# Kernel tuning notes

Hardware: AMD Instinct MI355X
Metric: run time of the kernel (lower is better)

## Reference

```python
import jax, jax.numpy as jnp
import numpy as np

N = 50000          # nodes
E = 800000         # directed edges (avg degree 16)
IN_F = 1433        # Cora num_features
N_CLS = 7          # Cora num_classes
HEADS = 8
HID = 32
NEG_SLOPE = 0.2    # PyG GATConv default negative_slope


def gat_conv(x, src, dst, W, a_src, a_dst, bias, heads, out_ch):
    """PyG GATConv (concat=True, add_self_loops=True, eval mode)."""
    n = x.shape[0]
    h = (x @ W).reshape(n, heads, out_ch)            # [N, H, C]
    # add self loops (PyG default)
    loop = jnp.arange(n, dtype=src.dtype)
    src = jnp.concatenate([src, loop])
    dst = jnp.concatenate([dst, loop])
    # attention logits per edge: a_src . h_src + a_dst . h_dst
    alpha_src = (h * a_src).sum(-1)                  # [N, H]
    alpha_dst = (h * a_dst).sum(-1)                  # [N, H]
    e = jax.nn.leaky_relu(alpha_src[src] + alpha_dst[dst], NEG_SLOPE)  # [E+N, H]
    # segment softmax over incoming edges of each destination node
    m = jax.ops.segment_max(e, dst, num_segments=n)  # [N, H]
    p = jnp.exp(e - m[dst])
    denom = jax.ops.segment_sum(p, dst, num_segments=n)
    alpha = p / denom[dst]                           # [E+N, H]
    # attention-weighted scatter-aggregate of source features
    out = jax.ops.segment_sum(h[src] * alpha[:, :, None], dst, num_segments=n)  # [N, H, C]
    return out.reshape(n, heads * out_ch) + bias


def setup_inputs() -> dict:
    key = jax.random.key(0)
    ks = jax.random.split(key, 12)
    s = 0.05
    x = jax.random.normal(ks[0], (N, IN_F), dtype=jnp.float32)
    edge_index = jax.random.randint(ks[1], (2, E), 0, N, dtype=jnp.int32)
    W1 = jax.random.normal(ks[2], (IN_F, HEADS * HID), dtype=jnp.float32) * s
    att_src1 = jax.random.normal(ks[3], (HEADS, HID), dtype=jnp.float32) * s
    att_dst1 = jax.random.normal(ks[4], (HEADS, HID), dtype=jnp.float32) * s
    bias1 = jnp.zeros((HEADS * HID,), dtype=jnp.float32)
    W2 = jax.random.normal(ks[5], (HEADS * HID, HEADS * N_CLS), dtype=jnp.float32) * s
    att_src2 = jax.random.normal(ks[6], (HEADS, N_CLS), dtype=jnp.float32) * s
    att_dst2 = jax.random.normal(ks[7], (HEADS, N_CLS), dtype=jnp.float32) * s
    bias2 = jnp.zeros((HEADS * N_CLS,), dtype=jnp.float32)
    return {
        "x": x, "edge_index": edge_index,
        "W1": W1, "att_src1": att_src1, "att_dst1": att_dst1, "bias1": bias1,
        "W2": W2, "att_src2": att_src2, "att_dst2": att_dst2, "bias2": bias2,
    }


def reference(x, edge_index, W1, att_src1, att_dst1, bias1,
              W2, att_src2, att_dst2, bias2):
    src, dst = edge_index[0], edge_index[1]
    # dropout (p=0.6) is identity in eval mode
    h = gat_conv(x, src, dst, W1, att_src1, att_dst1, bias1, HEADS, HID)
    h = jax.nn.elu(h)
    out = gat_conv(h, src, dst, W2, att_src2, att_dst2, bias2, HEADS, N_CLS)
    return out  # [N, HEADS * N_CLS]
```

## Files before the change

### kernel.cpp

```cpp
#include <hip/hip_runtime.h>
#include <math.h>

typedef short s16x8 __attribute__((ext_vector_type(8)));
typedef float f32x4 __attribute__((ext_vector_type(4)));

#define SLOPE 0.2f
#define K1 1433
#define KP 1440
#define NKB 45

static __device__ __forceinline__ float leaky(float x) {
  return x > 0.f ? x : SLOPE * x;
}

static __device__ __forceinline__ unsigned short f2bf(float f) {
  unsigned u = __builtin_bit_cast(unsigned, f);
  u += 0x7FFFu + ((u >> 16) & 1u);
  return (unsigned short)(u >> 16);
}
static __device__ __forceinline__ float bf2f(unsigned short h) {
  unsigned u = ((unsigned)h) << 16;
  return __builtin_bit_cast(float, u);
}

__global__ void w1t_kernel(const float* __restrict__ W1,
                           unsigned short* __restrict__ w1f) {
  int tid = blockIdx.x * 256 + threadIdx.x;
  if (tid >= NKB * 16 * 64) return;
  int l = tid & 63;
  int chunk = tid >> 6;
  int ntg = chunk & 15;
  int kb = chunk >> 4;
  int n = ntg * 16 + (l & 15);
  int kbase = kb * 32 + (l >> 4) * 8;
  unsigned short o[8];
#pragma unroll
  for (int e = 0; e < 8; ++e) {
    int k = kbase + e;
    float v = (k < K1) ? W1[(long)k * 256 + n] : 0.f;
    o[e] = f2bf(v);
  }
  *(ulonglong2*)(w1f + (long)tid * 8) = *(ulonglong2*)o;
}

__global__ __launch_bounds__(256, 3) void gemm1_mfma_kernel(
    const float* __restrict__ A, const unsigned short* __restrict__ w1f,
    float* __restrict__ C, int M) {
  __shared__ unsigned short As[2][4 * 2 * 64 * 8];
  __shared__ unsigned short Bs[2][16 * 64 * 8];
  const int t = threadIdx.x;
  const int w = t >> 6, l = t & 63;
  const int row0 = blockIdx.x * 64;

  f32x4 acc[4][4];
#pragma unroll
  for (int mt = 0; mt < 4; ++mt)
#pragma unroll
    for (int nt = 0; nt < 4; ++nt)
#pragma unroll
      for (int r = 0; r < 4; ++r) acc[mt][nt][r] = 0.f;

  const int sr = t >> 2, sg = t & 3;
  const int smt = sr >> 4, slr = sr & 15;
  const int lane_dst = slr + 16 * sg;
  const bool rowok = (row0 + sr) < M;
  const float* arow = A + (long)(row0 + sr) * K1;

  float v[8];

#pragma unroll
  for (int q = 0; q < 4; ++q) {
    int ng = w * 4 + q;
    const unsigned short* gsrc = w1f + (((long)0 * 16 + ng) * 64 + l) * 8;
    unsigned short* ldst = &Bs[0][ng * 512];
    __builtin_amdgcn_global_load_lds(
        (const __attribute__((address_space(1))) unsigned int*)gsrc,
        (__attribute__((address_space(3))) unsigned int*)ldst, 16, 0, 0);
  }
  {
    int kbase = sg * 8;
#pragma unroll
    for (int i = 0; i < 8; ++i) {
      int gk = kbase + i;
      v[i] = (rowok && gk < K1) ? arow[gk] : 0.f;
    }
    unsigned short hv[8], lv[8];
#pragma unroll
    for (int e = 0; e < 8; ++e) {
      unsigned short h = f2bf(v[e]);
      hv[e] = h;
      lv[e] = f2bf(v[e] - bf2f(h));
    }
    *(ulonglong2*)&As[0][((smt * 2 + 0) * 64 + lane_dst) * 8] = *(ulonglong2*)hv;
    *(ulonglong2*)&As[0][((smt * 2 + 1) * 64 + lane_dst) * 8] = *(ulonglong2*)lv;
  }
  __syncthreads();

  int cur = 0;
  for (int kb = 0; kb < NKB; ++kb) {
    const int nxt = kb + 1;
    if (nxt < NKB) {
#pragma unroll
      for (int q = 0; q < 4; ++q) {
        int ng = w * 4 + q;
        const unsigned short* gsrc =
            w1f + (((long)nxt * 16 + ng) * 64 + l) * 8;
        unsigned short* ldst = &Bs[cur ^ 1][ng * 512];
        __builtin_amdgcn_global_load_lds(
            (const __attribute__((address_space(1))) unsigned int*)gsrc,
            (__attribute__((address_space(3))) unsigned int*)ldst, 16, 0, 0);
      }
      int kbase = nxt * 32 + sg * 8;
#pragma unroll
      for (int i = 0; i < 8; ++i) {
        int gk = kbase + i;
        v[i] = (rowok && gk < K1) ? arow[gk] : 0.f;
      }
    }
    {
      s16x8 ah[4], al[4], bh[4];
#pragma unroll
      for (int mt = 0; mt < 4; ++mt) {
        ah[mt] = *(const s16x8*)&As[cur][(mt * 2 + 0) * 512 + l * 8];
        al[mt] = *(const s16x8*)&As[cur][(mt * 2 + 1) * 512 + l * 8];
      }
#pragma unroll
      for (int nt = 0; nt < 4; ++nt)
        bh[nt] = *(const s16x8*)&Bs[cur][(w * 4 + nt) * 512 + l * 8];
#pragma unroll
      for (int nt = 0; nt < 4; ++nt)
#pragma unroll
        for (int mt = 0; mt < 4; ++mt) {
          acc[mt][nt] = __builtin_amdgcn_mfma_f32_16x16x32_bf16(
              ah[mt], bh[nt], acc[mt][nt], 0, 0, 0);
          acc[mt][nt] = __builtin_amdgcn_mfma_f32_16x16x32_bf16(
              al[mt], bh[nt], acc[mt][nt], 0, 0, 0);
        }
    }
    if (nxt < NKB) {
      unsigned short hv[8], lv[8];
#pragma unroll
      for (int e = 0; e < 8; ++e) {
        unsigned short h = f2bf(v[e]);
        hv[e] = h;
        lv[e] = f2bf(v[e] - bf2f(h));
      }
      *(ulonglong2*)&As[cur ^ 1][((smt * 2 + 0) * 64 + lane_dst) * 8] =
          *(ulonglong2*)hv;
      *(ulonglong2*)&As[cur ^ 1][((smt * 2 + 1) * 64 + lane_dst) * 8] =
          *(ulonglong2*)lv;
      __syncthreads();
    }
    cur ^= 1;
  }
  const int crow4 = (l >> 4) * 4;
  const int ccol = l & 15;
#pragma unroll
  for (int mt = 0; mt < 4; ++mt) {
#pragma unroll
    for (int r = 0; r < 4; ++r) {
      int grow = row0 + mt * 16 + crow4 + r;
      if (grow < M) {
#pragma unroll
        for (int nt = 0; nt < 4; ++nt) {
          int gcol = w * 64 + nt * 16 + ccol;
          C[(long)grow * 256 + gcol] = acc[mt][nt][r];
        }
      }
    }
  }
}

__global__ void alpha1_kernel(const float* __restrict__ h1,
    const float* __restrict__ a_src, const float* __restrict__ a_dst,
    float* __restrict__ as_o, float* __restrict__ ad_o,
    unsigned short* __restrict__ h1b, int N) {
  int i = blockIdx.x * blockDim.x + threadIdx.x;
  if (i >= N * 8) return;
  int h = i & 7;
  const float* hp = h1 + (long)(i >> 3) * 256 + h * 32;
  const float* sp = a_src + h * 32;
  const float* dp = a_dst + h * 32;
  unsigned short ob[32];
  float s1 = 0.f, s2 = 0.f;
#pragma unroll
  for (int c = 0; c < 32; c += 4) {
    float4 v = *(const float4*)(hp + c);
    float4 ws = *(const float4*)(sp + c);
    float4 wd = *(const float4*)(dp + c);
    s1 += v.x * ws.x + v.y * ws.y + v.z * ws.z + v.w * ws.w;
    s2 += v.x * wd.x + v.y * wd.y + v.z * wd.z + v.w * wd.w;
    ob[c] = f2bf(v.x); ob[c + 1] = f2bf(v.y);
    ob[c + 2] = f2bf(v.z); ob[c + 3] = f2bf(v.w);
  }
  as_o[i] = s1;
  ad_o[i] = s2;
  unsigned short* op = h1b + (long)(i >> 3) * 256 + h * 32;
#pragma unroll
  for (int c = 0; c < 32; c += 8)
    *(ulonglong2*)(op + c) = *(ulonglong2*)(ob + c);
}

__global__ void hist_kernel(const int* __restrict__ dst, int* __restrict__ cnt,
                            int E, int N) {
  int e = blockIdx.x * blockDim.x + threadIdx.x;
  if (e >= E + N) return;
  int d = (e < E) ? dst[e] : (e - E);
  atomicAdd(&cnt[d], 1);
}

__global__ __launch_bounds__(1024) void scan_kernel(
    const int* __restrict__ cnt, int* __restrict__ rowptr,
    int* __restrict__ cursor, int N) {
  __shared__ int part[1024];
  const int tid = threadIdx.x;
  const int chunk = (N + 1023) / 1024;
  const int base = tid * chunk;
  const int lim = min(base + chunk, N);
  int sum = 0;
  for (int i = base; i < lim; ++i) sum += cnt[i];
  part[tid] = sum;
  __syncthreads();
  for (int off = 1; off < 1024; off <<= 1) {
    int v = (tid >= off) ? part[tid - off] : 0;
    __syncthreads();
    part[tid] += v;
    __syncthreads();
  }
  int run = (tid == 0) ? 0 : part[tid - 1];
  for (int i = base; i < lim; ++i) {
    rowptr[i] = run;
    cursor[i] = run;
    run += cnt[i];
  }
  if (tid == 1023) rowptr[N] = part[1023];
}

__global__ void scatter_kernel(const int* __restrict__ src,
    const int* __restrict__ dst, int* __restrict__ cursor,
    int* __restrict__ csr_src, int E, int N) {
  int e = blockIdx.x * blockDim.x + threadIdx.x;
  if (e >= E + N) return;
  int s, d;
  if (e < E) { s = src[e]; d = dst[e]; } else { s = e - E; d = s; }
  int pos = atomicAdd(&cursor[d], 1);
  csr_src[pos] = s;
}

__global__ __launch_bounds__(256) void agg1_fused_kernel(
    const int* __restrict__ rowptr, const int* __restrict__ csr_src,
    const float* __restrict__ as_, const float* __restrict__ ad_,
    const unsigned short* __restrict__ h1b, const float* __restrict__ bias,
    float* __restrict__ act, int N) {
  int d = blockIdx.x * 4 + (threadIdx.x >> 6);
  if (d >= N) return;
  int l = threadIdx.x & 63;
  int h = l >> 3;
  int rs = rowptr[d], re = rowptr[d + 1];
  float adv = ad_[d * 8 + h];
  float4 acc = make_float4(0.f, 0.f, 0.f, 0.f);
  float den = 0.f;
  for (int i = rs; i < re; ++i) {
    int s = csr_src[i];
    float a = __expf(leaky(as_[s * 8 + h] + adv));
    den += a;
    ushort4 u = *(const ushort4*)(h1b + (long)s * 256 + l * 4);
    acc.x += a * bf2f(u.x); acc.y += a * bf2f(u.y);
    acc.z += a * bf2f(u.z); acc.w += a * bf2f(u.w);
  }
  float inv = 1.f / den;
  float4 b = *(const float4*)(bias + l * 4);
  float4 o;
  o.x = acc.x * inv + b.x; o.y = acc.y * inv + b.y;
  o.z = acc.z * inv + b.z; o.w = acc.w * inv + b.w;
  o.x = o.x > 0.f ? o.x : expm1f(o.x);
  o.y = o.y > 0.f ? o.y : expm1f(o.y);
  o.z = o.z > 0.f ? o.z : expm1f(o.z);
  o.w = o.w > 0.f ? o.w : expm1f(o.w);
  *(float4*)(act + (long)d * 256 + l * 4) = o;
}

__global__ __launch_bounds__(256) void gemm2_kernel(const float* __restrict__ act,
    const float* __restrict__ W2, const float* __restrict__ a_src2,
    const float* __restrict__ a_dst2, unsigned short* __restrict__ h2b,
    float* __restrict__ as_o, float* __restrict__ ad_o, int N) {
  __shared__ float Ws[256 * 56];
  for (int i = threadIdx.x; i < 256 * 56; i += 256) Ws[i] = W2[i];
  __syncthreads();
  int n = blockIdx.x * 32 + (threadIdx.x >> 3);
  int h = threadIdx.x & 7;
  if (n >= N) return;
  const float* ap = act + (long)n * 256;
  float acc[7] = {0.f, 0.f, 0.f, 0.f, 0.f, 0.f, 0.f};
  for (int k0 = 0; k0 < 256; k0 += 4) {
    float4 a = *(const float4*)(ap + k0);
    float av[4] = {a.x, a.y, a.z, a.w};
#pragma unroll
    for (int kk = 0; kk < 4; ++kk) {
      const float* wp = &Ws[(k0 + kk) * 56 + h * 7];
#pragma unroll
      for (int j = 0; j < 7; ++j) acc[j] += av[kk] * wp[j];
    }
  }
  unsigned short* hp = h2b + (long)n * 56 + h * 7;
  float s1 = 0.f, s2 = 0.f;
#pragma unroll
  for (int j = 0; j < 7; ++j) {
    hp[j] = f2bf(acc[j]);
    s1 += acc[j] * a_src2[h * 7 + j];
    s2 += acc[j] * a_dst2[h * 7 + j];
  }
  as_o[n * 8 + h] = s1;
  ad_o[n * 8 + h] = s2;
}

__global__ __launch_bounds__(256) void agg2_fused_kernel(
    const int* __restrict__ rowptr, const int* __restrict__ csr_src,
    const float* __restrict__ as_, const float* __restrict__ ad_,
    const unsigned short* __restrict__ h2b, const float* __restrict__ bias,
    float* __restrict__ out, int N) {
  int d = blockIdx.x * 4 + (threadIdx.x >> 6);
  if (d >= N) return;
  int l = threadIdx.x & 63;
  int h = l >> 3, j = l & 7;
  int rs = rowptr[d], re = rowptr[d + 1];
  float adv = ad_[d * 8 + h];
  float acc = 0.f, den = 0.f;
  for (int i = rs; i < re; ++i) {
    int s = csr_src[i];
    float a = __expf(leaky(as_[s * 8 + h] + adv));
    den += a;
    if (j < 7) acc += a * bf2f(h2b[(long)s * 56 + h * 7 + j]);
  }
  if (j < 7) out[(long)d * 56 + h * 7 + j] = acc / den + bias[h * 7 + j];
}

extern "C" void kernel_launch(void* const* d_in, const int* in_sizes, int n_in,
                              void* d_out, int out_size, void* d_ws, size_t ws_size,
                              hipStream_t stream) {
  const float* x    = (const float*)d_in[0];
  const int*   ei   = (const int*)d_in[1];
  const float* W1   = (const float*)d_in[2];
  const float* asr1 = (const float*)d_in[3];
  const float* adt1 = (const float*)d_in[4];
  const float* b1   = (const float*)d_in[5];
  const float* W2   = (const float*)d_in[6];
  const float* asr2 = (const float*)d_in[7];
  const float* adt2 = (const float*)d_in[8];
  const float* b2   = (const float*)d_in[9];
  float* out = (float*)d_out;

  const int N = in_sizes[0] / K1;
  const int E = in_sizes[1] / 2;
  const int* src = ei;
  const int* dst = ei + E;

  float* ws = (float*)d_ws;
  float* h1  = ws; ws += (long)N * 256;
  float* act = ws; ws += (long)N * 256;
  float* as1 = ws; ws += N * 8;
  float* ad1 = ws; ws += N * 8;
  float* as2 = ws; ws += N * 8;
  float* ad2 = ws; ws += N * 8;
  unsigned short* h1b = (unsigned short*)ws; ws += (long)N * 128;
  unsigned short* h2b = (unsigned short*)ws; ws += (long)N * 28;
  unsigned short* w1f = (unsigned short*)ws; ws += NKB * 16 * 64 * 8 / 2;
  int* cnt     = (int*)ws; ws += N;
  int* rowptr  = (int*)ws; ws += N + 1;
  int* cursor  = (int*)ws; ws += N;
  int* csr_src = (int*)ws; ws += E + N;

  hipMemsetAsync(cnt, 0, (size_t)N * sizeof(int), stream);

  dim3 blk(256);

  hist_kernel<<<dim3((E + N + 255) / 256), blk, 0, stream>>>(dst, cnt, E, N);
  scan_kernel<<<dim3(1), dim3(1024), 0, stream>>>(cnt, rowptr, cursor, N);
  scatter_kernel<<<dim3((E + N + 255) / 256), blk, 0, stream>>>(
      src, dst, cursor, csr_src, E, N);
  {
    int tot = NKB * 16 * 64;
    w1t_kernel<<<dim3((tot + 255) / 256), blk, 0, stream>>>(W1, w1f);
  }

  gemm1_mfma_kernel<<<dim3((N + 63) / 64), blk, 0, stream>>>(x, w1f, h1, N);
  alpha1_kernel<<<dim3((N * 8 + 255) / 256), blk, 0, stream>>>(
      h1, asr1, adt1, as1, ad1, h1b, N);
  agg1_fused_kernel<<<dim3((N + 3) / 4), blk, 0, stream>>>(
      rowptr, csr_src, as1, ad1, h1b, b1, act, N);
  gemm2_kernel<<<dim3((N + 31) / 32), blk, 0, stream>>>(
      act, W2, asr2, adt2, h2b, as2, ad2, N);
  agg2_fused_kernel<<<dim3((N + 3) / 4), blk, 0, stream>>>(
      rowptr, csr_src, as2, ad2, h2b, b2, out, N);
}
```

Before: 727.1 us.

## Load GEMM1 A operand directly into registers and prefetch CSR neighbors in aggregation

The layer-1 GEMM stops staging the fp32 activations through shared memory. Each lane now loads its A fragment straight from global memory as float4, splits it into bf16 hi/lo in registers, and feeds the MFMAs directly. Warps are retiled 2x2 (32 rows x 128 cols each) so A fragments are reused across 8 N-tiles, and the K loop is unrolled by two with register double buffering. The aggregation kernels software-prefetch the next source index and its attention logit to hide the dependent-load latency, at the cost of a few more registers.

```diff
diff --git a/kernel.cpp b/kernel.cpp
--- a/kernel.cpp
+++ b/kernel.cpp
@@ -46,124 +46,114 @@
 __global__ __launch_bounds__(256, 3) void gemm1_mfma_kernel(
     const float* __restrict__ A, const unsigned short* __restrict__ w1f,
     float* __restrict__ C, int M) {
-  __shared__ unsigned short As[2][4 * 2 * 64 * 8];
   __shared__ unsigned short Bs[2][16 * 64 * 8];
   const int t = threadIdx.x;
   const int w = t >> 6, l = t & 63;
+  const int wm = w >> 1, wn = w & 1;
   const int row0 = blockIdx.x * 64;
-
-  f32x4 acc[4][4];
-#pragma unroll
-  for (int mt = 0; mt < 4; ++mt)
-#pragma unroll
-    for (int nt = 0; nt < 4; ++nt)
+  const int lrow = l & 15, lkg = l >> 4;
+
+  f32x4 acc[2][8];
+#pragma unroll
+  for (int mt = 0; mt < 2; ++mt)
+#pragma unroll
+    for (int nt = 0; nt < 8; ++nt)
 #pragma unroll
       for (int r = 0; r < 4; ++r) acc[mt][nt][r] = 0.f;
 
-  const int sr = t >> 2, sg = t & 3;
-  const int smt = sr >> 4, slr = sr & 15;
-  const int lane_dst = slr + 16 * sg;
-  const bool rowok = (row0 + sr) < M;
-  const float* arow = A + (long)(row0 + sr) * K1;
-
-  float v[8];
-
-#pragma unroll
-  for (int q = 0; q < 4; ++q) {
-    int ng = w * 4 + q;
-    const unsigned short* gsrc = w1f + (((long)0 * 16 + ng) * 64 + l) * 8;
-    unsigned short* ldst = &Bs[0][ng * 512];
-    __builtin_amdgcn_global_load_lds(
-        (const __attribute__((address_space(1))) unsigned int*)gsrc,
-        (__attribute__((address_space(3))) unsigned int*)ldst, 16, 0, 0);
-  }
-  {
-    int kbase = sg * 8;
-#pragma unroll
-    for (int i = 0; i < 8; ++i) {
-      int gk = kbase + i;
-      v[i] = (rowok && gk < K1) ? arow[gk] : 0.f;
-    }
-    unsigned short hv[8], lv[8];
+  const int r0 = row0 + wm * 32 + lrow;
+  const int r1 = r0 + 16;
+  const bool ok0 = r0 < M, ok1 = r1 < M;
+  const float* a0 = A + (long)(ok0 ? r0 : 0) * K1 + lkg * 8;
+  const float* a1 = A + (long)(ok1 ? r1 : 0) * K1 + lkg * 8;
+  const float4 f4z = make_float4(0.f, 0.f, 0.f, 0.f);
+
+  auto stage = [&](int kb, int buf) {
+#pragma unroll
+    for (int q = 0; q < 4; ++q) {
+      int ng = w * 4 + q;
+      const unsigned short* gsrc = w1f + (((long)kb * 16 + ng) * 64 + l) * 8;
+      unsigned short* ldst = &Bs[buf][ng * 512];
+      __builtin_amdgcn_global_load_lds(
+          (const __attribute__((address_space(1))) unsigned int*)gsrc,
+          (__attribute__((address_space(3))) unsigned int*)ldst, 16, 0, 0);
+    }
+  };
+
+  auto loada = [&](int kb, float4* v) {
+    if (kb < NKB - 1) {
+      v[0] = ok0 ? *(const float4*)(a0 + kb * 32) : f4z;
+      v[1] = ok0 ? *(const float4*)(a0 + kb * 32 + 4) : f4z;
+      v[2] = ok1 ? *(const float4*)(a1 + kb * 32) : f4z;
+      v[3] = ok1 ? *(const float4*)(a1 + kb * 32 + 4) : f4z;
+    } else {
+      if (lkg < 3) {
+        v[0] = ok0 ? *(const float4*)(a0 + kb * 32) : f4z;
+        v[1] = ok0 ? *(const float4*)(a0 + kb * 32 + 4) : f4z;
+        v[2] = ok1 ? *(const float4*)(a1 + kb * 32) : f4z;
+        v[3] = ok1 ? *(const float4*)(a1 + kb * 32 + 4) : f4z;
+      } else {
+        v[0] = f4z; v[1] = f4z; v[2] = f4z; v[3] = f4z;
+        v[0].x = ok0 ? a0[kb * 32] : 0.f;
+        v[2].x = ok1 ? a1[kb * 32] : 0.f;
+      }
+    }
+  };
+
+  auto cvt2 = [&](const float4& x, const float4& y, s16x8& ah, s16x8& al) {
+    float f[8] = {x.x, x.y, x.z, x.w, y.x, y.y, y.z, y.w};
 #pragma unroll
     for (int e = 0; e < 8; ++e) {
-      unsigned short h = f2bf(v[e]);
-      hv[e] = h;
-      lv[e] = f2bf(v[e] - bf2f(h));
-    }
-    *(ulonglong2*)&As[0][((smt * 2 + 0) * 64 + lane_dst) * 8] = *(ulonglong2*)hv;
-    *(ulonglong2*)&As[0][((smt * 2 + 1) * 64 + lane_dst) * 8] = *(ulonglong2*)lv;
-  }
+      unsigned short h = f2bf(f[e]);
+      ah[e] = (short)h;
+      al[e] = (short)f2bf(f[e] - bf2f(h));
+    }
+  };
+
+  auto compute = [&](int cur, const float4* v) {
+    s16x8 ah0, al0, ah1, al1;
+    cvt2(v[0], v[1], ah0, al0);
+    cvt2(v[2], v[3], ah1, al1);
+    const unsigned short* bp = &Bs[cur][wn * 8 * 512 + l * 8];
+#pragma unroll
+    for (int nt = 0; nt < 8; ++nt) {
+      s16x8 bh = *(const s16x8*)(bp + nt * 512);
+      acc[0][nt] = __builtin_amdgcn_mfma_f32_16x16x32_bf16(ah0, bh, acc[0][nt], 0, 0, 0);
+      acc[0][nt] = __builtin_amdgcn_mfma_f32_16x16x32_bf16(al0, bh, acc[0][nt], 0, 0, 0);
+      acc[1][nt] = __builtin_amdgcn_mfma_f32_16x16x32_bf16(ah1, bh, acc[1][nt], 0, 0, 0);
+      acc[1][nt] = __builtin_amdgcn_mfma_f32_16x16x32_bf16(al1, bh, acc[1][nt], 0, 0, 0);
+    }
+  };
+
+  float4 vA[4], vB[4];
+  stage(0, 0);
+  loada(0, vA);
   __syncthreads();
 
-  int cur = 0;
-  for (int kb = 0; kb < NKB; ++kb) {
-    const int nxt = kb + 1;
-    if (nxt < NKB) {
-#pragma unroll
-      for (int q = 0; q < 4; ++q) {
-        int ng = w * 4 + q;
-        const unsigned short* gsrc =
-            w1f + (((long)nxt * 16 + ng) * 64 + l) * 8;
-        unsigned short* ldst = &Bs[cur ^ 1][ng * 512];
-        __builtin_amdgcn_global_load_lds(
-            (const __attribute__((address_space(1))) unsigned int*)gsrc,
-            (__attribute__((address_space(3))) unsigned int*)ldst, 16, 0, 0);
-      }
-      int kbase = nxt * 32 + sg * 8;
-#pragma unroll
-      for (int i = 0; i < 8; ++i) {
-        int gk = kbase + i;
-        v[i] = (rowok && gk < K1) ? arow[gk] : 0.f;
-      }
-    }
-    {
-      s16x8 ah[4], al[4], bh[4];
-#pragma unroll
-      for (int mt = 0; mt < 4; ++mt) {
-        ah[mt] = *(const s16x8*)&As[cur][(mt * 2 + 0) * 512 + l * 8];
-        al[mt] = *(const s16x8*)&As[cur][(mt * 2 + 1) * 512 + l * 8];
-      }
-#pragma unroll
-      for (int nt = 0; nt < 4; ++nt)
-        bh[nt] = *(const s16x8*)&Bs[cur][(w * 4 + nt) * 512 + l * 8];
-#pragma unroll
-      for (int nt = 0; nt < 4; ++nt)
-#pragma unroll
-        for (int mt = 0; mt < 4; ++mt) {
-          acc[mt][nt] = __builtin_amdgcn_mfma_f32_16x16x32_bf16(
-              ah[mt], bh[nt], acc[mt][nt], 0, 0, 0);
-          acc[mt][nt] = __builtin_amdgcn_mfma_f32_16x16x32_bf16(
-              al[mt], bh[nt], acc[mt][nt], 0, 0, 0);
-        }
-    }
-    if (nxt < NKB) {
-      unsigned short hv[8], lv[8];
-#pragma unroll
-      for (int e = 0; e < 8; ++e) {
-        unsigned short h = f2bf(v[e]);
-        hv[e] = h;
-        lv[e] = f2bf(v[e] - bf2f(h));
-      }
-      *(ulonglong2*)&As[cur ^ 1][((smt * 2 + 0) * 64 + lane_dst) * 8] =
-          *(ulonglong2*)hv;
-      *(ulonglong2*)&As[cur ^ 1][((smt * 2 + 1) * 64 + lane_dst) * 8] =
-          *(ulonglong2*)lv;
-      __syncthreads();
-    }
-    cur ^= 1;
-  }
+  for (int kb = 0; kb < NKB - 1; kb += 2) {
+    stage(kb + 1, 1);
+    loada(kb + 1, vB);
+    compute(0, vA);
+    __syncthreads();
+    if (kb + 2 < NKB) {
+      stage(kb + 2, 0);
+      loada(kb + 2, vA);
+    }
+    compute(1, vB);
+    __syncthreads();
+  }
+  compute(0, vA);
+
   const int crow4 = (l >> 4) * 4;
-  const int ccol = l & 15;
-#pragma unroll
-  for (int mt = 0; mt < 4; ++mt) {
+#pragma unroll
+  for (int mt = 0; mt < 2; ++mt) {
 #pragma unroll
     for (int r = 0; r < 4; ++r) {
-      int grow = row0 + mt * 16 + crow4 + r;
+      int grow = row0 + wm * 32 + mt * 16 + crow4 + r;
       if (grow < M) {
 #pragma unroll
-        for (int nt = 0; nt < 4; ++nt) {
-          int gcol = w * 64 + nt * 16 + ccol;
+        for (int nt = 0; nt < 8; ++nt) {
+          int gcol = wn * 128 + nt * 16 + lrow;
           C[(long)grow * 256 + gcol] = acc[mt][nt][r];
         }
       }
@@ -260,11 +250,18 @@
   float adv = ad_[d * 8 + h];
   float4 acc = make_float4(0.f, 0.f, 0.f, 0.f);
   float den = 0.f;
+  int sN = csr_src[rs];
+  float asN = as_[sN * 8 + h];
   for (int i = rs; i < re; ++i) {
-    int s = csr_src[i];
-    float a = __expf(leaky(as_[s * 8 + h] + adv));
+    int sC = sN;
+    float asC = asN;
+    if (i + 1 < re) {
+      sN = csr_src[i + 1];
+      asN = as_[sN * 8 + h];
+    }
+    float a = __expf(leaky(asC + adv));
+    ushort4 u = *(const ushort4*)(h1b + (long)sC * 256 + l * 4);
     den += a;
-    ushort4 u = *(const ushort4*)(h1b + (long)s * 256 + l * 4);
     acc.x += a * bf2f(u.x); acc.y += a * bf2f(u.y);
     acc.z += a * bf2f(u.z); acc.w += a * bf2f(u.w);
   }
@@ -326,11 +323,18 @@
   int rs = rowptr[d], re = rowptr[d + 1];
   float adv = ad_[d * 8 + h];
   float acc = 0.f, den = 0.f;
+  int sN = csr_src[rs];
+  float asN = as_[sN * 8 + h];
   for (int i = rs; i < re; ++i) {
-    int s = csr_src[i];
-    float a = __expf(leaky(as_[s * 8 + h] + adv));
+    int sC = sN;
+    float asC = asN;
+    if (i + 1 < re) {
+      sN = csr_src[i + 1];
+      asN = as_[sN * 8 + h];
+    }
+    float a = __expf(leaky(asC + adv));
     den += a;
-    if (j < 7) acc += a * bf2f(h2b[(long)s * 56 + h * 7 + j]);
+    if (j < 7) acc += a * bf2f(h2b[(long)sC * 56 + h * 7 + j]);
   }
   if (j < 7) out[(long)d * 56 + h * 7 + j] = acc / den + bias[h * 7 + j];
 }
```

Measured after the change: 805.7 us. +10.8%, slower.
